# Kernel tuning notes

Measured on AMD Instinct MI355X. Metric: run time of the kernel, lower is better.

The kernel has to match this reference:

```python
import jax, jax.numpy as jnp
import numpy as np

B, S, D = 2, 1024, 768
H, HD = 12, 64
E, K, F = 8, 2, 3072
EPS = 1e-5


def _ln(x, g, b):
    mu = jnp.mean(x, -1, keepdims=True)
    var = jnp.mean(jnp.square(x - mu), -1, keepdims=True)
    return (x - mu) * jax.lax.rsqrt(var + EPS) * g + b


def setup_inputs() -> dict:
    key = jax.random.key(0)
    ks = jax.random.split(key, 12)
    s = lambda k, shape, sc: jax.random.normal(k, shape, jnp.float32) * sc
    return {
        "hidden_states": s(ks[0], (B, S, D), 1.0),
        "ln1_g": jnp.ones((D,), jnp.float32), "ln1_b": jnp.zeros((D,), jnp.float32),
        "w_attn": s(ks[1], (D, 3 * D), 0.02), "b_attn": jnp.zeros((3 * D,), jnp.float32),
        "w_attnproj": s(ks[2], (D, D), 0.02), "b_attnproj": jnp.zeros((D,), jnp.float32),
        "ln2_g": jnp.ones((D,), jnp.float32), "ln2_b": jnp.zeros((D,), jnp.float32),
        "w_router": s(ks[3], (E, D), 0.01),
        "w_fc": s(ks[4], (E, D, F), 0.02 / E), "b_fc": jnp.zeros((E, F), jnp.float32),
        "w_proj": s(ks[5], (E, F, D), 0.02 / E), "b_proj": jnp.zeros((E, D), jnp.float32),
    }


def reference(hidden_states, ln1_g, ln1_b, w_attn, b_attn, w_attnproj, b_attnproj,
              ln2_g, ln2_b, w_router, w_fc, b_fc, w_proj, b_proj):
    # --- attention sub-block (GPT-2 style, causal) ---
    residual = hidden_states
    x = _ln(hidden_states, ln1_g, ln1_b)
    qkv = x @ w_attn + b_attn                         # [B,S,3D]
    q, k, v = jnp.split(qkv, 3, axis=-1)
    def heads(t):
        return t.reshape(B, S, H, HD).transpose(0, 2, 1, 3)  # [B,H,S,HD]
    q, k, v = heads(q), heads(k), heads(v)
    scores = jnp.einsum("bhqd,bhkd->bhqk", q, k) / np.sqrt(HD).astype(np.float32)
    causal = jnp.tril(jnp.ones((S, S), bool))
    scores = jnp.where(causal, scores, jnp.finfo(scores.dtype).min)
    attn = jax.nn.softmax(scores, axis=-1)
    ctx = jnp.einsum("bhqk,bhkd->bhqd", attn, v)
    ctx = ctx.transpose(0, 2, 1, 3).reshape(B, S, D)
    attn_out = ctx @ w_attnproj + b_attnproj
    hs = attn_out + residual

    # --- MoE FFN sub-block ---
    residual = hs
    x2 = _ln(hs, ln2_g, ln2_b)
    logits = x2 @ w_router.T                          # [B,S,E]
    probs = jax.nn.softmax(logits, axis=-1)
    top_w, top_idx = jax.lax.top_k(probs, K)          # [B,S,K]
    top_w = top_w / jnp.sum(top_w, -1, keepdims=True)
    gates = jnp.sum(jax.nn.one_hot(top_idx, E, dtype=x2.dtype) * top_w[..., None], axis=2)  # [B,S,E]
    h = jax.nn.gelu(jnp.einsum("bsd,edf->bsef", x2, w_fc) + b_fc, approximate=False)
    y = jnp.einsum("bsef,efd->bsed", h, w_proj) + b_proj
    moe_out = jnp.einsum("bse,bsed->bsd", gates, y)
    return moe_out + residual
```

## Files before the change

kernel.cpp:

```cpp
#include <hip/hip_runtime.h>
#include <hip/hip_bf16.h>
#include <math.h>

#define NB 2
#define SEQ 1024
#define DM 768
#define NHEAD 12
#define HDIM 64
#define NEXP 8
#define FF 3072
#define NTOK (NB*SEQ)
#define TDIM (3*DM)
#define LNEPS 1e-5f
#define NSLOT (NTOK*2)

typedef __attribute__((ext_vector_type(8))) short v8s;
typedef __attribute__((ext_vector_type(4))) float v4f;

#define GLDS16(src, dst) \
    __builtin_amdgcn_global_load_lds((const __attribute__((address_space(1))) unsigned int*)(src), \
                                     (__attribute__((address_space(3))) unsigned int*)(dst), 16, 0, 0)

#define BARF() do { asm volatile("" ::: "memory"); __builtin_amdgcn_s_barrier(); asm volatile("" ::: "memory"); } while(0)
#define WAITV(n) asm volatile("s_waitcnt vmcnt(" #n ")" ::: "memory")

static __device__ __forceinline__ float bf2f(unsigned short u){
    return __uint_as_float(((unsigned)u) << 16);
}
static __device__ __forceinline__ unsigned short f2bf(float f){
    unsigned u = __float_as_uint(f);
    u += 0x7fffu + ((u >> 16) & 1u);
    return (unsigned short)(u >> 16);
}
static __device__ __forceinline__ float gelu_exact(float x){
    return 0.5f * x * (1.0f + erff(x * 0.70710678118654752440f));
}

__global__ __launch_bounds__(256) void tconv_kernel(const float* __restrict__ in,
                                                    unsigned short* __restrict__ out,
                                                    int R, int C){
    __shared__ float T[32][33];
    size_t base = (size_t)blockIdx.z * R * C;
    int c0 = blockIdx.x * 32, r0 = blockIdx.y * 32;
    int t = threadIdx.x;
    int tr = t >> 3, tc4 = (t & 7) * 4;
    float4 v = *(const float4*)&in[base + (size_t)(r0 + tr) * C + c0 + tc4];
    T[tr][tc4+0] = v.x; T[tr][tc4+1] = v.y; T[tr][tc4+2] = v.z; T[tr][tc4+3] = v.w;
    __syncthreads();
    int oc = t >> 3, or4 = (t & 7) * 4;
    ushort4 o;
    o.x = f2bf(T[or4+0][oc]); o.y = f2bf(T[or4+1][oc]);
    o.z = f2bf(T[or4+2][oc]); o.w = f2bf(T[or4+3][oc]);
    *(ushort4*)&out[base + (size_t)(c0 + oc) * R + r0 + or4] = o;
}

__global__ __launch_bounds__(256) void ln_b(const float* __restrict__ in,
                                            const float* __restrict__ g,
                                            const float* __restrict__ b,
                                            unsigned short* __restrict__ outb){
    int t = blockIdx.x;
    const float* row = in + (size_t)t * DM;
    int tid = threadIdx.x;
    float v0 = row[tid], v1 = row[tid + 256], v2 = row[tid + 512];
    float s  = v0 + v1 + v2;
    float ss = v0*v0 + v1*v1 + v2*v2;
    for (int off = 32; off; off >>= 1){
        s  += __shfl_down(s, off);
        ss += __shfl_down(ss, off);
    }
    __shared__ float ls[4], lss[4];
    int wid = tid >> 6, lane = tid & 63;
    if (lane == 0){ ls[wid] = s; lss[wid] = ss; }
    __syncthreads();
    if (tid == 0){
        float a = ls[0] + ls[1] + ls[2] + ls[3];
        float c = lss[0] + lss[1] + lss[2] + lss[3];
        float mu = a / (float)DM;
        float var = c / (float)DM - mu * mu;
        ls[0] = mu; lss[0] = rsqrtf(var + LNEPS);
    }
    __syncthreads();
    float mu = ls[0], rs = lss[0];
    unsigned short* obrow = outb + (size_t)t * DM;
    obrow[tid]     = f2bf((v0 - mu) * rs * g[tid]       + b[tid]);
    obrow[tid+256] = f2bf((v1 - mu) * rs * g[tid + 256] + b[tid + 256]);
    obrow[tid+512] = f2bf((v2 - mu) * rs * g[tid + 512] + b[tid + 512]);
}

__global__ __launch_bounds__(256) void ln_router(const float* __restrict__ in,
                                                 const float* __restrict__ g,
                                                 const float* __restrict__ b,
                                                 const float* __restrict__ wr,
                                                 unsigned short* __restrict__ outb,
                                                 int* __restrict__ cnt,
                                                 int* __restrict__ expTok,
                                                 int* __restrict__ tokE,
                                                 int* __restrict__ tokPos,
                                                 float* __restrict__ tokGate){
    int t = blockIdx.x;
    const float* row = in + (size_t)t * DM;
    int tid = threadIdx.x;
    float v0 = row[tid], v1 = row[tid + 256], v2 = row[tid + 512];
    float s  = v0 + v1 + v2;
    float ss = v0*v0 + v1*v1 + v2*v2;
    for (int off = 32; off; off >>= 1){
        s  += __shfl_down(s, off);
        ss += __shfl_down(ss, off);
    }
    __shared__ float ls[4], lss[4];
    __shared__ float wsum[4][NEXP];
    int wid = tid >> 6, lane = tid & 63;
    if (lane == 0){ ls[wid] = s; lss[wid] = ss; }
    __syncthreads();
    if (tid == 0){
        float a = ls[0] + ls[1] + ls[2] + ls[3];
        float c = lss[0] + lss[1] + lss[2] + lss[3];
        float mu = a / (float)DM;
        float var = c / (float)DM - mu * mu;
        ls[0] = mu; lss[0] = rsqrtf(var + LNEPS);
    }
    __syncthreads();
    float mu = ls[0], rs = lss[0];
    float o0 = (v0 - mu) * rs * g[tid]       + b[tid];
    float o1 = (v1 - mu) * rs * g[tid + 256] + b[tid + 256];
    float o2 = (v2 - mu) * rs * g[tid + 512] + b[tid + 512];
    unsigned short* obrow = outb + (size_t)t * DM;
    obrow[tid] = f2bf(o0); obrow[tid+256] = f2bf(o1); obrow[tid+512] = f2bf(o2);
    float p[NEXP];
    #pragma unroll
    for (int e = 0; e < NEXP; e++)
        p[e] = o0*wr[e*DM + tid] + o1*wr[e*DM + tid + 256] + o2*wr[e*DM + tid + 512];
    #pragma unroll
    for (int e = 0; e < NEXP; e++)
        for (int off = 32; off; off >>= 1) p[e] += __shfl_down(p[e], off);
    if (lane == 0){
        #pragma unroll
        for (int e = 0; e < NEXP; e++) wsum[wid][e] = p[e];
    }
    __syncthreads();
    if (tid == 0){
        float lg[NEXP];
        #pragma unroll
        for (int e = 0; e < NEXP; e++)
            lg[e] = wsum[0][e] + wsum[1][e] + wsum[2][e] + wsum[3][e];
        int i0 = 0; float m0 = lg[0];
        #pragma unroll
        for (int e = 1; e < NEXP; e++) if (lg[e] > m0){ m0 = lg[e]; i0 = e; }
        int i1 = -1; float m1 = -INFINITY;
        #pragma unroll
        for (int e = 0; e < NEXP; e++) if (e != i0 && lg[e] > m1){ m1 = lg[e]; i1 = e; }
        float mx = fmaxf(m0, m1);
        float e0 = __expf(m0 - mx), e1 = __expf(m1 - mx);
        float inv = 1.0f / (e0 + e1);
        int p0 = atomicAdd(&cnt[i0], 1);
        int p1 = atomicAdd(&cnt[i1], 1);
        expTok[i0*NTOK + p0] = t;
        expTok[i1*NTOK + p1] = t;
        tokE[t*2]   = i0; tokE[t*2+1]   = i1;
        tokPos[t*2] = p0; tokPos[t*2+1] = p1;
        tokGate[t*2]   = e0 * inv;
        tokGate[t*2+1] = e1 * inv;
    }
}

__global__ __launch_bounds__(256) void mm_qkv(const unsigned short* __restrict__ Ab,
                                              const unsigned short* __restrict__ Bb,
                                              const float* __restrict__ bias,
                                              unsigned short* __restrict__ Qb,
                                              unsigned short* __restrict__ Kb,
                                              unsigned short* __restrict__ Vt){
    __shared__ __align__(16) unsigned short As[2][64*32];
    __shared__ __align__(16) unsigned short Bs[2][64*32];
    int bm = blockIdx.y * 64, bn = blockIdx.x * 64;
    int tid = threadIdx.x, wave = tid >> 6, lane = tid & 63;
    int quad = lane >> 4, l15 = lane & 15;
    int wm = wave >> 1, wn = wave & 1;
    int arow = tid >> 2, achunk = (tid & 3) * 8;
    const unsigned short* aS = Ab + (size_t)(bm + arow) * DM + achunk;
    const unsigned short* bS = Bb + (size_t)(bn + arow) * DM + achunk;
    v4f acc[2][2];
    #pragma unroll
    for (int i = 0; i < 2; i++)
        #pragma unroll
        for (int j = 0; j < 2; j++) acc[i][j] = (v4f){0.f,0.f,0.f,0.f};

#define QKV_STAGE(buf, kt) do { int kb = (kt)*32; \
    GLDS16(aS + kb, &As[buf][(wave*16)*32]); \
    GLDS16(bS + kb, &Bs[buf][(wave*16)*32]); \
} while(0)
#define QKV_COMP(buf) do { \
    v8s a[2], bfr[2]; \
    _Pragma("unroll") \
    for (int i = 0; i < 2; i++){ \
        a[i]   = *(const v8s*)&As[buf][(wm*32 + i*16 + l15)*32 + quad*8]; \
        bfr[i] = *(const v8s*)&Bs[buf][(wn*32 + i*16 + l15)*32 + quad*8]; \
    } \
    _Pragma("unroll") \
    for (int mi = 0; mi < 2; mi++) \
        _Pragma("unroll") \
        for (int ni = 0; ni < 2; ni++) \
            acc[mi][ni] = __builtin_amdgcn_mfma_f32_16x16x32_bf16(a[mi], bfr[ni], acc[mi][ni], 0, 0, 0); \
} while(0)

    const int NK = DM/32;
    QKV_STAGE(0, 0);
    #pragma unroll 1
    for (int kt = 0; kt < NK; kt++){
        if (NK - kt > 1){ QKV_STAGE((kt+1)&1, kt+1); WAITV(2); }
        else            { WAITV(0); }
        BARF();
        QKV_COMP(kt&1);
        BARF();
    }
    int btyp = bn / DM;
    #pragma unroll
    for (int ni = 0; ni < 2; ni++){
        int n = bn + wn*32 + ni*16 + l15;
        float bb = bias[n];
        int hd = n % DM; int h = hd >> 6; int d = hd & 63;
        #pragma unroll
        for (int mi = 0; mi < 2; mi++){
            int m = bm + wm*32 + mi*16 + quad*4;
            int b = m >> 10, sd = m & 1023;
            size_t bhbase = (size_t)(b*NHEAD + h);
            if (btyp == 0){
                #pragma unroll
                for (int r = 0; r < 4; r++)
                    Qb[(bhbase*SEQ + sd + r)*HDIM + d] = f2bf((acc[mi][ni][r] + bb) * 0.125f);
            } else if (btyp == 1){
                #pragma unroll
                for (int r = 0; r < 4; r++)
                    Kb[(bhbase*SEQ + sd + r)*HDIM + d] = f2bf(acc[mi][ni][r] + bb);
            } else {
                ushort4 o;
                o.x = f2bf(acc[mi][ni][0] + bb); o.y = f2bf(acc[mi][ni][1] + bb);
                o.z = f2bf(acc[mi][ni][2] + bb); o.w = f2bf(acc[mi][ni][3] + bb);
                *(ushort4*)&Vt[(bhbase*HDIM + d)*SEQ + sd] = o;
            }
        }
    }
}

__global__ __launch_bounds__(64) void fattn(const unsigned short* __restrict__ Qb,
                                            const unsigned short* __restrict__ Kb,
                                            const unsigned short* __restrict__ Vt,
                                            unsigned short* __restrict__ ctxb){
    int bh = blockIdx.x >> 5;
    int q0 = (31 - (blockIdx.x & 31)) * 32;
    int h = bh % NHEAD, b = bh / NHEAD;
    int lane = threadIdx.x;
    int quad = lane >> 4, l15 = lane & 15;

    __shared__ __align__(16) unsigned short Plds[32*32];

    const unsigned short* qp = Qb + ((size_t)bh*SEQ + q0 + l15) * HDIM + quad*8;
    v8s qa00 = *(const v8s*)qp;
    v8s qa01 = *(const v8s*)(qp + 32);
    v8s qa10 = *(const v8s*)(qp + 16*HDIM);
    v8s qa11 = *(const v8s*)(qp + 16*HDIM + 32);

    v4f o[2][4];
    #pragma unroll
    for (int i = 0; i < 2; i++)
        #pragma unroll
        for (int j = 0; j < 4; j++) o[i][j] = (v4f){0.f,0.f,0.f,0.f};
    float mrow[2][4], lrow[2][4];
    #pragma unroll
    for (int i = 0; i < 2; i++)
        #pragma unroll
        for (int r = 0; r < 4; r++){ mrow[i][r] = -1e30f; lrow[i][r] = 0.f; }

    int nch = (q0 >> 5) + 1;
    for (int ch = 0; ch < nch; ch++){
        int kt = ch * 32;
        const unsigned short* kp = Kb + ((size_t)bh*SEQ + kt + l15) * HDIM + quad*8;
        v8s k00 = *(const v8s*)kp;
        v8s k01 = *(const v8s*)(kp + 32);
        v8s k10 = *(const v8s*)(kp + 16*HDIM);
        v8s k11 = *(const v8s*)(kp + 16*HDIM + 32);
        v4f s00 = {0,0,0,0}, s01 = {0,0,0,0}, s10 = {0,0,0,0}, s11 = {0,0,0,0};
        s00 = __builtin_amdgcn_mfma_f32_16x16x32_bf16(qa00, k00, s00, 0, 0, 0);
        s00 = __builtin_amdgcn_mfma_f32_16x16x32_bf16(qa01, k01, s00, 0, 0, 0);
        s01 = __builtin_amdgcn_mfma_f32_16x16x32_bf16(qa00, k10, s01, 0, 0, 0);
        s01 = __builtin_amdgcn_mfma_f32_16x16x32_bf16(qa01, k11, s01, 0, 0, 0);
        s10 = __builtin_amdgcn_mfma_f32_16x16x32_bf16(qa10, k00, s10, 0, 0, 0);
        s10 = __builtin_amdgcn_mfma_f32_16x16x32_bf16(qa11, k01, s10, 0, 0, 0);
        s11 = __builtin_amdgcn_mfma_f32_16x16x32_bf16(qa10, k10, s11, 0, 0, 0);
        s11 = __builtin_amdgcn_mfma_f32_16x16x32_bf16(qa11, k11, s11, 0, 0, 0);

        int key0 = kt + l15, key1 = kt + 16 + l15;
        float alpha[2][4];
        #pragma unroll
        for (int mi = 0; mi < 2; mi++){
            #pragma unroll
            for (int r = 0; r < 4; r++){
                int qrow = q0 + mi*16 + quad*4 + r;
                float sv0 = mi ? s10[r] : s00[r];
                float sv1 = mi ? s11[r] : s01[r];
                float v0 = (key0 <= qrow) ? sv0 : -1e30f;
                float v1 = (key1 <= qrow) ? sv1 : -1e30f;
                float mx = fmaxf(v0, v1);
                mx = fmaxf(mx, __shfl_xor(mx, 1));
                mx = fmaxf(mx, __shfl_xor(mx, 2));
                mx = fmaxf(mx, __shfl_xor(mx, 4));
                mx = fmaxf(mx, __shfl_xor(mx, 8));
                float mn = fmaxf(mrow[mi][r], mx);
                alpha[mi][r] = __expf(mrow[mi][r] - mn);
                float p0 = __expf(v0 - mn);
                float p1 = __expf(v1 - mn);
                float ps = p0 + p1;
                ps += __shfl_xor(ps, 1);
                ps += __shfl_xor(ps, 2);
                ps += __shfl_xor(ps, 4);
                ps += __shfl_xor(ps, 8);
                lrow[mi][r] = lrow[mi][r] * alpha[mi][r] + ps;
                mrow[mi][r] = mn;
                Plds[(mi*16 + quad*4 + r)*32 + l15]      = f2bf(p0);
                Plds[(mi*16 + quad*4 + r)*32 + 16 + l15] = f2bf(p1);
            }
        }
        #pragma unroll
        for (int mi = 0; mi < 2; mi++)
            #pragma unroll
            for (int df = 0; df < 4; df++)
                #pragma unroll
                for (int r = 0; r < 4; r++)
                    o[mi][df][r] *= alpha[mi][r];
        __syncthreads();
        v8s pa0 = *(const v8s*)&Plds[l15*32 + quad*8];
        v8s pa1 = *(const v8s*)&Plds[(16 + l15)*32 + quad*8];
        const unsigned short* vp = Vt + ((size_t)bh*HDIM + l15) * SEQ + kt + quad*8;
        #pragma unroll
        for (int df = 0; df < 4; df++){
            v8s vb = *(const v8s*)(vp + df*16*SEQ);
            o[0][df] = __builtin_amdgcn_mfma_f32_16x16x32_bf16(pa0, vb, o[0][df], 0, 0, 0);
            o[1][df] = __builtin_amdgcn_mfma_f32_16x16x32_bf16(pa1, vb, o[1][df], 0, 0, 0);
        }
        __syncthreads();
    }
    #pragma unroll
    for (int mi = 0; mi < 2; mi++){
        #pragma unroll
        for (int r = 0; r < 4; r++){
            float inv = 1.0f / lrow[mi][r];
            size_t orow = (size_t)(b*SEQ + q0 + mi*16 + quad*4 + r) * DM + h*HDIM;
            #pragma unroll
            for (int df = 0; df < 4; df++)
                ctxb[orow + df*16 + l15] = f2bf(o[mi][df][r] * inv);
        }
    }
}

__global__ __launch_bounds__(256) void mm_attnproj(const unsigned short* __restrict__ Ab,
                                                   const unsigned short* __restrict__ Bb,
                                                   const float* __restrict__ bias,
                                                   const float* __restrict__ res,
                                                   float* __restrict__ C){
    __shared__ __align__(16) unsigned short As[4][64*32];
    __shared__ __align__(16) unsigned short Bs[4][64*32];
    int bm = blockIdx.y * 64, bn = blockIdx.x * 64;
    int tid = threadIdx.x, wave = tid >> 6, lane = tid & 63;
    int quad = lane >> 4, l15 = lane & 15;
    int wm = wave >> 1, wn = wave & 1;
    int lrow = lane >> 2, lchunk = (lane & 3) * 8;
    const unsigned short* aS = Ab + (size_t)(bm + wave*16 + lrow) * DM + lchunk;
    const unsigned short* bS = Bb + (size_t)(bn + wave*16 + lrow) * DM + lchunk;
    v4f acc[2][2];
    #pragma unroll
    for (int i = 0; i < 2; i++)
        #pragma unroll
        for (int j = 0; j < 2; j++) acc[i][j] = (v4f){0.f,0.f,0.f,0.f};

#define AP_STAGE(buf, kt) do { int kb = (kt)*32; \
    GLDS16(aS + kb, &As[buf][(wave*16)*32]); \
    GLDS16(bS + kb, &Bs[buf][(wave*16)*32]); \
} while(0)
#define AP_COMP(buf) do { \
    v8s a[2], bfr[2]; \
    _Pragma("unroll") \
    for (int i = 0; i < 2; i++){ \
        a[i]   = *(const v8s*)&As[buf][(wm*32 + i*16 + l15)*32 + quad*8]; \
        bfr[i] = *(const v8s*)&Bs[buf][(wn*32 + i*16 + l15)*32 + quad*8]; \
    } \
    _Pragma("unroll") \
    for (int mi = 0; mi < 2; mi++) \
        _Pragma("unroll") \
        for (int ni = 0; ni < 2; ni++) \
            acc[mi][ni] = __builtin_amdgcn_mfma_f32_16x16x32_bf16(a[mi], bfr[ni], acc[mi][ni], 0, 0, 0); \
} while(0)

    const int NK = DM/32;
    AP_STAGE(0, 0); AP_STAGE(1, 1); AP_STAGE(2, 2);
    #pragma unroll 1
    for (int kt = 0; kt < NK; kt++){
        int rem = NK - kt;
        if (rem > 3){ AP_STAGE((kt+3)&3, kt+3); WAITV(6); }
        else if (rem == 3){ WAITV(4); }
        else if (rem == 2){ WAITV(2); }
        else { WAITV(0); }
        BARF();
        AP_COMP(kt&3);
        BARF();
    }
    #pragma unroll
    for (int ni = 0; ni < 2; ni++){
        int n = bn + wn*32 + ni*16 + l15;
        float bb = bias[n];
        #pragma unroll
        for (int mi = 0; mi < 2; mi++){
            int m = bm + wm*32 + mi*16 + quad*4;
            #pragma unroll
            for (int r = 0; r < 4; r++)
                C[(size_t)(m + r) * DM + n] = acc[mi][ni][r] + bb + res[(size_t)(m + r) * DM + n];
        }
    }
}

__global__ __launch_bounds__(256) void mm_fc(const unsigned short* __restrict__ Xb,
                                             const unsigned short* __restrict__ Wb,
                                             const float* __restrict__ bfc,
                                             const int* __restrict__ expTok,
                                             const int* __restrict__ cnt,
                                             const int* __restrict__ offE,
                                             unsigned short* __restrict__ H){
    int bid = blockIdx.x;
    int e = bid & 7;
    int t2 = bid >> 3;
    int tile = t2 & 31;
    int bn = (t2 >> 5) * 128;
    int c = cnt[e];
    int rows = c - tile * 64;
    if (rows <= 0) return;
    __shared__ __align__(16) unsigned short As[2][64*32];
    __shared__ __align__(16) unsigned short Bs[2][128*32];
    __shared__ int toks[64];
    int tid = threadIdx.x, wave = tid >> 6, lane = tid & 63;
    if (tid < 64){
        int idx = tile * 64 + tid;
        if (idx >= c) idx = c - 1;
        toks[tid] = expTok[e * NTOK + idx];
    }
    __syncthreads();
    int quad = lane >> 4, l15 = lane & 15;
    int wm = wave >> 1, wn = wave & 1;
    int lrow = lane >> 2;
    int pch = (((lane >> 3) & 3) ^ (lane & 3)) * 8;
    int tok0 = toks[wave*16 + lrow];
    const unsigned short* Be = Wb + (size_t)e * FF * DM;
    const unsigned short* aS  = Xb + (size_t)tok0 * DM + pch;
    const unsigned short* bS0 = Be + (size_t)(bn +      wave*16 + lrow) * DM + pch;
    const unsigned short* bS1 = Be + (size_t)(bn + 64 + wave*16 + lrow) * DM + pch;
    int q2 = (quad ^ ((l15 >> 1) & 3)) * 8;
    v4f acc[2][4];
    #pragma unroll
    for (int i = 0; i < 2; i++)
        #pragma unroll
        for (int j = 0; j < 4; j++) acc[i][j] = (v4f){0.f,0.f,0.f,0.f};

#define FC_STAGE(buf, kt) do { int kb = (kt)*32; \
    GLDS16(aS  + kb, &As[buf][(wave*16)*32]); \
    GLDS16(bS0 + kb, &Bs[buf][(     wave*16)*32]); \
    GLDS16(bS1 + kb, &Bs[buf][(64 + wave*16)*32]); \
} while(0)
#define FC_COMP(buf) do { \
    v8s a[2], bfr[4]; \
    _Pragma("unroll") \
    for (int i = 0; i < 2; i++) a[i] = *(const v8s*)&As[buf][(wm*32 + i*16 + l15)*32 + q2]; \
    _Pragma("unroll") \
    for (int i = 0; i < 4; i++) bfr[i] = *(const v8s*)&Bs[buf][(wn*64 + i*16 + l15)*32 + q2]; \
    _Pragma("unroll") \
    for (int mi = 0; mi < 2; mi++) \
        _Pragma("unroll") \
        for (int ni = 0; ni < 4; ni++) \
            acc[mi][ni] = __builtin_amdgcn_mfma_f32_16x16x32_bf16(a[mi], bfr[ni], acc[mi][ni], 0, 0, 0); \
} while(0)

    const int NK = DM/32;
    FC_STAGE(0, 0);
    #pragma unroll 1
    for (int kt = 0; kt < NK; kt++){
        if (NK - kt > 1){ FC_STAGE((kt+1)&1, kt+1); WAITV(3); }
        else            { WAITV(0); }
        BARF();
        FC_COMP(kt&1);
        BARF();
    }
    int slot0 = offE[e] + tile * 64;
    #pragma unroll
    for (int ni = 0; ni < 4; ni++){
        int n = bn + wn*64 + ni*16 + l15;
        float bb = bfc[(size_t)e * FF + n];
        #pragma unroll
        for (int mi = 0; mi < 2; mi++){
            int ml = wm*32 + mi*16 + quad*4;
            #pragma unroll
            for (int r = 0; r < 4; r++)
                if (ml + r < rows)
                    H[(size_t)(slot0 + ml + r) * FF + n] = f2bf(gelu_exact(acc[mi][ni][r] + bb));
        }
    }
}

__global__ __launch_bounds__(256) void mm_proj(const unsigned short* __restrict__ H,
                                               const unsigned short* __restrict__ Wb,
                                               const int* __restrict__ cnt,
                                               const int* __restrict__ offE,
                                               float* __restrict__ Yp){
    int bid = blockIdx.x;
    int e = bid & 7;
    int t2 = bid >> 3;
    int tile = t2 & 31;
    int xx = t2 >> 5;
    int sk = xx & 1;
    int bn = (xx >> 1) * 64;
    int c = cnt[e];
    int rows = c - tile * 64;
    if (rows <= 0) return;
    __shared__ __align__(16) unsigned short As[2][64*32];
    __shared__ __align__(16) unsigned short Bs[2][64*32];
    int tid = threadIdx.x, wave = tid >> 6, lane = tid & 63;
    int quad = lane >> 4, l15 = lane & 15;
    int wm = wave >> 1, wn = wave & 1;
    int slot0 = offE[e] + tile * 64;
    int arow = tid >> 2;
    int pch = (((lane >> 3) & 3) ^ (lane & 3)) * 8;
    int arl = arow < rows ? arow : rows - 1;
    const unsigned short* Be = Wb + (size_t)e * DM * FF;
    const unsigned short* aS = H  + (size_t)(slot0 + arl) * FF + sk*1536 + pch;
    const unsigned short* bS = Be + (size_t)(bn + arow) * FF + sk*1536 + pch;
    int q2 = (quad ^ ((l15 >> 1) & 3)) * 8;
    v4f acc[2][2];
    #pragma unroll
    for (int i = 0; i < 2; i++)
        #pragma unroll
        for (int j = 0; j < 2; j++) acc[i][j] = (v4f){0.f,0.f,0.f,0.f};

#define PJ_STAGE(buf, kt) do { int kb = (kt)*32; \
    GLDS16(aS + kb, &As[buf][(wave*16)*32]); \
    GLDS16(bS + kb, &Bs[buf][(wave*16)*32]); \
} while(0)
#define PJ_COMP(buf) do { \
    v8s a[2], bfr[2]; \
    _Pragma("unroll") \
    for (int i = 0; i < 2; i++){ \
        a[i]   = *(const v8s*)&As[buf][(wm*32 + i*16 + l15)*32 + q2]; \
        bfr[i] = *(const v8s*)&Bs[buf][(wn*32 + i*16 + l15)*32 + q2]; \
    } \
    _Pragma("unroll") \
    for (int mi = 0; mi < 2; mi++) \
        _Pragma("unroll") \
        for (int ni = 0; ni < 2; ni++) \
            acc[mi][ni] = __builtin_amdgcn_mfma_f32_16x16x32_bf16(a[mi], bfr[ni], acc[mi][ni], 0, 0, 0); \
} while(0)

    const int NK = 1536/32;
    PJ_STAGE(0, 0);
    #pragma unroll 1
    for (int kt = 0; kt < NK; kt++){
        if (NK - kt > 1){ PJ_STAGE((kt+1)&1, kt+1); WAITV(2); }
        else            { WAITV(0); }
        BARF();
        PJ_COMP(kt&1);
        BARF();
    }
    float* Yo = Yp + (size_t)sk * NSLOT * DM;
    #pragma unroll
    for (int ni = 0; ni < 2; ni++){
        int n = bn + wn*32 + ni*16 + l15;
        #pragma unroll
        for (int mi = 0; mi < 2; mi++){
            int ml = wm*32 + mi*16 + quad*4;
            #pragma unroll
            for (int r = 0; r < 4; r++)
                if (ml + r < rows)
                    Yo[(size_t)(slot0 + ml + r) * DM + n] = acc[mi][ni][r];
        }
    }
}

__global__ void offsets_kernel(const int* __restrict__ cnt, int* __restrict__ offE){
    if (threadIdx.x == 0 && blockIdx.x == 0){
        int a = 0;
        for (int e = 0; e < NEXP; e++){ offE[e] = a; a += cnt[e]; }
    }
}

__global__ __launch_bounds__(256) void combine_kernel(const float* __restrict__ hs,
                                                      const float* __restrict__ Yp,
                                                      const float* __restrict__ bproj,
                                                      const int* __restrict__ tokE,
                                                      const int* __restrict__ tokPos,
                                                      const float* __restrict__ tokGate,
                                                      const int* __restrict__ offE,
                                                      float* __restrict__ out){
    int t = blockIdx.x;
    int e0 = tokE[t*2], e1 = tokE[t*2+1];
    int s0 = offE[e0] + tokPos[t*2];
    int s1 = offE[e1] + tokPos[t*2+1];
    float g0 = tokGate[t*2], g1 = tokGate[t*2+1];
    const float* y0a = Yp + (size_t)s0 * DM;
    const float* y0b = Yp + (size_t)NSLOT * DM + (size_t)s0 * DM;
    const float* y1a = Yp + (size_t)s1 * DM;
    const float* y1b = Yp + (size_t)NSLOT * DM + (size_t)s1 * DM;
    const float* b0 = bproj + (size_t)e0 * DM;
    const float* b1 = bproj + (size_t)e1 * DM;
    const float* hr = hs + (size_t)t * DM;
    float* orow = out + (size_t)t * DM;
    for (int d = threadIdx.x; d < DM; d += 256){
        orow[d] = hr[d] + g0 * (y0a[d] + y0b[d] + b0[d]) + g1 * (y1a[d] + y1b[d] + b1[d]);
    }
}

extern "C" void kernel_launch(void* const* d_in, const int* in_sizes, int n_in,
                              void* d_out, int out_size, void* d_ws, size_t ws_size,
                              hipStream_t stream){
    (void)in_sizes; (void)n_in; (void)out_size; (void)ws_size;
    const float* hidden  = (const float*)d_in[0];
    const float* ln1_g   = (const float*)d_in[1];
    const float* ln1_b   = (const float*)d_in[2];
    const float* w_attn  = (const float*)d_in[3];
    const float* b_attn  = (const float*)d_in[4];
    const float* w_aproj = (const float*)d_in[5];
    const float* b_aproj = (const float*)d_in[6];
    const float* ln2_g   = (const float*)d_in[7];
    const float* ln2_b   = (const float*)d_in[8];
    const float* w_rout  = (const float*)d_in[9];
    const float* w_fc    = (const float*)d_in[10];
    const float* b_fc    = (const float*)d_in[11];
    const float* w_proj  = (const float*)d_in[12];
    const float* b_proj  = (const float*)d_in[13];
    float* out = (float*)d_out;

    char* ws = (char*)d_ws;
    float*          hs   = (float*)(ws + 0);
    unsigned short* xb   = (unsigned short*)(ws + 6291456);
    unsigned short* Qb   = (unsigned short*)(ws + 9437184);
    unsigned short* Kb   = (unsigned short*)(ws + 12582912);
    unsigned short* Vt   = (unsigned short*)(ws + 15728640);
    unsigned short* ctxb = (unsigned short*)(ws + 18874368);
    unsigned short* Wab  = (unsigned short*)(ws + 22020096);
    unsigned short* Wapb = (unsigned short*)(ws + 25559040);
    unsigned short* H    = (unsigned short*)(ws + 9437184);
    unsigned short* Wfcb = (unsigned short*)(ws + 34603008);
    unsigned short* Wprb = (unsigned short*)(ws + 72351744);
    float*          Yp   = (float*)(ws + 34603008);
    char* rt = ws + 110100480;
    int* cnt      = (int*)(rt + 0);
    int* offE     = (int*)(rt + 64);
    int* expTok   = (int*)(rt + 128);
    int* tokE     = (int*)(rt + 128 + 65536);
    int* tokPos   = (int*)(rt + 128 + 81920);
    float* tokGate= (float*)(rt + 128 + 98304);

    hipMemsetAsync(cnt, 0, NEXP * sizeof(int), stream);

    tconv_kernel<<<dim3(TDIM/32, DM/32, 1), 256, 0, stream>>>(w_attn, Wab, DM, TDIM);
    tconv_kernel<<<dim3(DM/32, DM/32, 1), 256, 0, stream>>>(w_aproj, Wapb, DM, DM);
    tconv_kernel<<<dim3(FF/32, DM/32, NEXP), 256, 0, stream>>>(w_fc, Wfcb, DM, FF);
    tconv_kernel<<<dim3(DM/32, FF/32, NEXP), 256, 0, stream>>>(w_proj, Wprb, FF, DM);

    ln_b<<<NTOK, 256, 0, stream>>>(hidden, ln1_g, ln1_b, xb);
    mm_qkv<<<dim3(TDIM/64, NTOK/64), 256, 0, stream>>>(xb, Wab, b_attn, Qb, Kb, Vt);
    fattn<<<NB*NHEAD*32, 64, 0, stream>>>(Qb, Kb, Vt, ctxb);
    mm_attnproj<<<dim3(DM/64, NTOK/64), 256, 0, stream>>>(ctxb, Wapb, b_aproj, hidden, hs);
    ln_router<<<NTOK, 256, 0, stream>>>(hs, ln2_g, ln2_b, w_rout, xb,
                                        cnt, expTok, tokE, tokPos, tokGate);
    offsets_kernel<<<1, 64, 0, stream>>>(cnt, offE);
    mm_fc<<<8 * (NTOK/64) * (FF/128), 256, 0, stream>>>(xb, Wfcb, b_fc, expTok, cnt, offE, H);
    mm_proj<<<8 * (NTOK/64) * ((DM/64)*2), 256, 0, stream>>>(H, Wprb, cnt, offE, Yp);
    combine_kernel<<<NTOK, 256, 0, stream>>>(hs, Yp, b_proj, tokE, tokPos, tokGate, offE, out);
}
```

Measured before the change: 496.6 us.

## Enlarge MoE FC and proj GEMM tiles to 256-row blocks with 512 threads

Rewrites the expert FC and projection GEMMs to use 256x256 (fc) and 256x128 (proj) block tiles with K-step 64, 8 waves per block, and an XOR-swizzled LDS layout. Token indices are now gathered directly per lane instead of through a shared toks array. The larger tiles raise arithmetic intensity and cut redundant weight and activation loads across blocks. In exchange, the kernels use much more LDS and more accumulator registers, and launch fewer blocks. That lowers occupancy and wastes work on partially filled 256-row expert tiles.

```diff
diff --git a/kernel.cpp b/kernel.cpp
--- a/kernel.cpp
+++ b/kernel.cpp
@@ -416,83 +416,88 @@
     }
 }
 
-__global__ __launch_bounds__(256) void mm_fc(const unsigned short* __restrict__ Xb,
-                                             const unsigned short* __restrict__ Wb,
-                                             const float* __restrict__ bfc,
-                                             const int* __restrict__ expTok,
-                                             const int* __restrict__ cnt,
-                                             const int* __restrict__ offE,
-                                             unsigned short* __restrict__ H){
+__global__ __launch_bounds__(512, 2) void mm_fc(const unsigned short* __restrict__ Xb,
+                                                const unsigned short* __restrict__ Wb,
+                                                const float* __restrict__ bfc,
+                                                const int* __restrict__ expTok,
+                                                const int* __restrict__ cnt,
+                                                const int* __restrict__ offE,
+                                                unsigned short* __restrict__ H){
     int bid = blockIdx.x;
     int e = bid & 7;
     int t2 = bid >> 3;
-    int tile = t2 & 31;
-    int bn = (t2 >> 5) * 128;
+    int mt = t2 & 7;
+    int bn = (t2 >> 3) * 256;
     int c = cnt[e];
-    int rows = c - tile * 64;
+    int rows = c - mt * 256;
     if (rows <= 0) return;
-    __shared__ __align__(16) unsigned short As[2][64*32];
-    __shared__ __align__(16) unsigned short Bs[2][128*32];
-    __shared__ int toks[64];
+    __shared__ __align__(16) unsigned short As[2][256*64];
+    __shared__ __align__(16) unsigned short Bs[2][256*64];
     int tid = threadIdx.x, wave = tid >> 6, lane = tid & 63;
-    if (tid < 64){
-        int idx = tile * 64 + tid;
-        if (idx >= c) idx = c - 1;
-        toks[tid] = expTok[e * NTOK + idx];
-    }
-    __syncthreads();
     int quad = lane >> 4, l15 = lane & 15;
-    int wm = wave >> 1, wn = wave & 1;
-    int lrow = lane >> 2;
-    int pch = (((lane >> 3) & 3) ^ (lane & 3)) * 8;
-    int tok0 = toks[wave*16 + lrow];
+    int wm = wave >> 2, wn = wave & 3;
+    int srow = lane >> 3;
+    int schunk = (lane & 7) ^ srow;
     const unsigned short* Be = Wb + (size_t)e * FF * DM;
-    const unsigned short* aS  = Xb + (size_t)tok0 * DM + pch;
-    const unsigned short* bS0 = Be + (size_t)(bn +      wave*16 + lrow) * DM + pch;
-    const unsigned short* bS1 = Be + (size_t)(bn + 64 + wave*16 + lrow) * DM + pch;
-    int q2 = (quad ^ ((l15 >> 1) & 3)) * 8;
-    v4f acc[2][4];
-    #pragma unroll
-    for (int i = 0; i < 2; i++)
+    const unsigned short* aSrc[4];
+    const unsigned short* bSrc[4];
+    #pragma unroll
+    for (int s = 0; s < 4; s++){
+        int arow = mt*256 + wave*32 + s*8 + srow;
+        if (arow >= c) arow = c - 1;
+        int tok = expTok[e*NTOK + arow];
+        aSrc[s] = Xb + (size_t)tok * DM + schunk*8;
+        bSrc[s] = Be + (size_t)(bn + wave*32 + s*8 + srow) * DM + schunk*8;
+    }
+    v4f acc[8][4];
+    #pragma unroll
+    for (int i = 0; i < 8; i++)
         #pragma unroll
         for (int j = 0; j < 4; j++) acc[i][j] = (v4f){0.f,0.f,0.f,0.f};
 
-#define FC_STAGE(buf, kt) do { int kb = (kt)*32; \
-    GLDS16(aS  + kb, &As[buf][(wave*16)*32]); \
-    GLDS16(bS0 + kb, &Bs[buf][(     wave*16)*32]); \
-    GLDS16(bS1 + kb, &Bs[buf][(64 + wave*16)*32]); \
-} while(0)
-#define FC_COMP(buf) do { \
-    v8s a[2], bfr[4]; \
-    _Pragma("unroll") \
-    for (int i = 0; i < 2; i++) a[i] = *(const v8s*)&As[buf][(wm*32 + i*16 + l15)*32 + q2]; \
-    _Pragma("unroll") \
-    for (int i = 0; i < 4; i++) bfr[i] = *(const v8s*)&Bs[buf][(wn*64 + i*16 + l15)*32 + q2]; \
-    _Pragma("unroll") \
-    for (int mi = 0; mi < 2; mi++) \
+#define FC_STG(buf, kt) do { int kb = (kt)*64; \
+    _Pragma("unroll") \
+    for (int s = 0; s < 4; s++){ \
+        GLDS16(aSrc[s] + kb, &As[buf][(wave*32 + s*8)*64]); \
+        GLDS16(bSrc[s] + kb, &Bs[buf][(wave*32 + s*8)*64]); \
+    } \
+} while(0)
+#define FC_CMP(buf) do { \
+    _Pragma("unroll") \
+    for (int h = 0; h < 2; h++){ \
+        v8s a[8], bq[4]; \
+        _Pragma("unroll") \
+        for (int mi = 0; mi < 8; mi++) \
+            a[mi] = *(const v8s*)&As[buf][(wm*128 + mi*16 + l15)*64 + ((h*4 + quad) ^ (l15 & 7))*8]; \
         _Pragma("unroll") \
         for (int ni = 0; ni < 4; ni++) \
-            acc[mi][ni] = __builtin_amdgcn_mfma_f32_16x16x32_bf16(a[mi], bfr[ni], acc[mi][ni], 0, 0, 0); \
-} while(0)
-
-    const int NK = DM/32;
-    FC_STAGE(0, 0);
+            bq[ni] = *(const v8s*)&Bs[buf][(wn*64 + ni*16 + l15)*64 + ((h*4 + quad) ^ (l15 & 7))*8]; \
+        _Pragma("unroll") \
+        for (int mi = 0; mi < 8; mi++) \
+            _Pragma("unroll") \
+            for (int ni = 0; ni < 4; ni++) \
+                acc[mi][ni] = __builtin_amdgcn_mfma_f32_16x16x32_bf16(a[mi], bq[ni], acc[mi][ni], 0, 0, 0); \
+    } \
+} while(0)
+
+    const int NK = DM/64;
+    FC_STG(0, 0);
     #pragma unroll 1
     for (int kt = 0; kt < NK; kt++){
-        if (NK - kt > 1){ FC_STAGE((kt+1)&1, kt+1); WAITV(3); }
+        if (kt + 1 < NK){ FC_STG((kt+1)&1, kt+1); WAITV(8); }
         else            { WAITV(0); }
         BARF();
-        FC_COMP(kt&1);
-        BARF();
-    }
-    int slot0 = offE[e] + tile * 64;
+        FC_CMP(kt&1);
+        BARF();
+    }
+    int slot0 = offE[e] + mt*256;
     #pragma unroll
     for (int ni = 0; ni < 4; ni++){
         int n = bn + wn*64 + ni*16 + l15;
         float bb = bfc[(size_t)e * FF + n];
         #pragma unroll
-        for (int mi = 0; mi < 2; mi++){
-            int ml = wm*32 + mi*16 + quad*4;
+        for (int mi = 0; mi < 8; mi++){
+            int ml = wm*128 + mi*16 + quad*4;
             #pragma unroll
             for (int r = 0; r < 4; r++)
                 if (ml + r < rows)
@@ -501,75 +506,90 @@
     }
 }
 
-__global__ __launch_bounds__(256) void mm_proj(const unsigned short* __restrict__ H,
-                                               const unsigned short* __restrict__ Wb,
-                                               const int* __restrict__ cnt,
-                                               const int* __restrict__ offE,
-                                               float* __restrict__ Yp){
+__global__ __launch_bounds__(512, 2) void mm_proj(const unsigned short* __restrict__ H,
+                                                  const unsigned short* __restrict__ Wb,
+                                                  const int* __restrict__ cnt,
+                                                  const int* __restrict__ offE,
+                                                  float* __restrict__ Yp){
     int bid = blockIdx.x;
     int e = bid & 7;
     int t2 = bid >> 3;
-    int tile = t2 & 31;
-    int xx = t2 >> 5;
-    int sk = xx & 1;
-    int bn = (xx >> 1) * 64;
+    int mt = t2 & 7;
+    int t3 = t2 >> 3;
+    int sk = t3 & 1;
+    int bn = (t3 >> 1) * 128;
     int c = cnt[e];
-    int rows = c - tile * 64;
+    int rows = c - mt * 256;
     if (rows <= 0) return;
-    __shared__ __align__(16) unsigned short As[2][64*32];
-    __shared__ __align__(16) unsigned short Bs[2][64*32];
+    __shared__ __align__(16) unsigned short As[2][256*64];
+    __shared__ __align__(16) unsigned short Bs[2][128*64];
     int tid = threadIdx.x, wave = tid >> 6, lane = tid & 63;
     int quad = lane >> 4, l15 = lane & 15;
     int wm = wave >> 1, wn = wave & 1;
-    int slot0 = offE[e] + tile * 64;
-    int arow = tid >> 2;
-    int pch = (((lane >> 3) & 3) ^ (lane & 3)) * 8;
-    int arl = arow < rows ? arow : rows - 1;
+    int slot0 = offE[e] + mt*256;
+    int srow = lane >> 3;
+    int schunk = (lane & 7) ^ srow;
     const unsigned short* Be = Wb + (size_t)e * DM * FF;
-    const unsigned short* aS = H  + (size_t)(slot0 + arl) * FF + sk*1536 + pch;
-    const unsigned short* bS = Be + (size_t)(bn + arow) * FF + sk*1536 + pch;
-    int q2 = (quad ^ ((l15 >> 1) & 3)) * 8;
-    v4f acc[2][2];
-    #pragma unroll
-    for (int i = 0; i < 2; i++)
-        #pragma unroll
-        for (int j = 0; j < 2; j++) acc[i][j] = (v4f){0.f,0.f,0.f,0.f};
-
-#define PJ_STAGE(buf, kt) do { int kb = (kt)*32; \
-    GLDS16(aS + kb, &As[buf][(wave*16)*32]); \
-    GLDS16(bS + kb, &Bs[buf][(wave*16)*32]); \
-} while(0)
-#define PJ_COMP(buf) do { \
-    v8s a[2], bfr[2]; \
-    _Pragma("unroll") \
-    for (int i = 0; i < 2; i++){ \
-        a[i]   = *(const v8s*)&As[buf][(wm*32 + i*16 + l15)*32 + q2]; \
-        bfr[i] = *(const v8s*)&Bs[buf][(wn*32 + i*16 + l15)*32 + q2]; \
+    const unsigned short* aSrc[4];
+    const unsigned short* bSrc[2];
+    #pragma unroll
+    for (int s = 0; s < 4; s++){
+        int arow = wave*32 + s*8 + srow;
+        if (arow >= rows) arow = rows - 1;
+        aSrc[s] = H + (size_t)(slot0 + arow) * FF + sk*1536 + schunk*8;
+    }
+    #pragma unroll
+    for (int s = 0; s < 2; s++)
+        bSrc[s] = Be + (size_t)(bn + wave*16 + s*8 + srow) * FF + sk*1536 + schunk*8;
+    v4f acc[4][4];
+    #pragma unroll
+    for (int i = 0; i < 4; i++)
+        #pragma unroll
+        for (int j = 0; j < 4; j++) acc[i][j] = (v4f){0.f,0.f,0.f,0.f};
+
+#define PJ_STG(buf, kt) do { int kb = (kt)*64; \
+    _Pragma("unroll") \
+    for (int s = 0; s < 4; s++) \
+        GLDS16(aSrc[s] + kb, &As[buf][(wave*32 + s*8)*64]); \
+    _Pragma("unroll") \
+    for (int s = 0; s < 2; s++) \
+        GLDS16(bSrc[s] + kb, &Bs[buf][(wave*16 + s*8)*64]); \
+} while(0)
+#define PJ_CMP(buf) do { \
+    _Pragma("unroll") \
+    for (int h = 0; h < 2; h++){ \
+        v8s a[4], bq[4]; \
+        _Pragma("unroll") \
+        for (int mi = 0; mi < 4; mi++) \
+            a[mi] = *(const v8s*)&As[buf][(wm*64 + mi*16 + l15)*64 + ((h*4 + quad) ^ (l15 & 7))*8]; \
+        _Pragma("unroll") \
+        for (int ni = 0; ni < 4; ni++) \
+            bq[ni] = *(const v8s*)&Bs[buf][(wn*64 + ni*16 + l15)*64 + ((h*4 + quad) ^ (l15 & 7))*8]; \
+        _Pragma("unroll") \
+        for (int mi = 0; mi < 4; mi++) \
+            _Pragma("unroll") \
+            for (int ni = 0; ni < 4; ni++) \
+                acc[mi][ni] = __builtin_amdgcn_mfma_f32_16x16x32_bf16(a[mi], bq[ni], acc[mi][ni], 0, 0, 0); \
     } \
-    _Pragma("unroll") \
-    for (int mi = 0; mi < 2; mi++) \
-        _Pragma("unroll") \
-        for (int ni = 0; ni < 2; ni++) \
-            acc[mi][ni] = __builtin_amdgcn_mfma_f32_16x16x32_bf16(a[mi], bfr[ni], acc[mi][ni], 0, 0, 0); \
-} while(0)
-
-    const int NK = 1536/32;
-    PJ_STAGE(0, 0);
+} while(0)
+
+    const int NK = 1536/64;
+    PJ_STG(0, 0);
     #pragma unroll 1
     for (int kt = 0; kt < NK; kt++){
-        if (NK - kt > 1){ PJ_STAGE((kt+1)&1, kt+1); WAITV(2); }
+        if (kt + 1 < NK){ PJ_STG((kt+1)&1, kt+1); WAITV(6); }
         else            { WAITV(0); }
         BARF();
-        PJ_COMP(kt&1);
+        PJ_CMP(kt&1);
         BARF();
     }
     float* Yo = Yp + (size_t)sk * NSLOT * DM;
     #pragma unroll
-    for (int ni = 0; ni < 2; ni++){
-        int n = bn + wn*32 + ni*16 + l15;
-        #pragma unroll
-        for (int mi = 0; mi < 2; mi++){
-            int ml = wm*32 + mi*16 + quad*4;
+    for (int ni = 0; ni < 4; ni++){
+        int n = bn + wn*64 + ni*16 + l15;
+        #pragma unroll
+        for (int mi = 0; mi < 4; mi++){
+            int ml = wm*64 + mi*16 + quad*4;
             #pragma unroll
             for (int r = 0; r < 4; r++)
                 if (ml + r < rows)
@@ -666,7 +686,7 @@
     ln_router<<<NTOK, 256, 0, stream>>>(hs, ln2_g, ln2_b, w_rout, xb,
                                         cnt, expTok, tokE, tokPos, tokGate);
     offsets_kernel<<<1, 64, 0, stream>>>(cnt, offE);
-    mm_fc<<<8 * (NTOK/64) * (FF/128), 256, 0, stream>>>(xb, Wfcb, b_fc, expTok, cnt, offE, H);
-    mm_proj<<<8 * (NTOK/64) * ((DM/64)*2), 256, 0, stream>>>(H, Wprb, cnt, offE, Yp);
+    mm_fc<<<8 * 8 * (FF/256), 512, 0, stream>>>(xb, Wfcb, b_fc, expTok, cnt, offE, H);
+    mm_proj<<<8 * 8 * 2 * (DM/128), 512, 0, stream>>>(H, Wprb, cnt, offE, Yp);
     combine_kernel<<<NTOK, 256, 0, stream>>>(hs, Yp, b_proj, tokE, tokPos, tokGate, offE, out);
 }
```

Result: slower. 534.2 us (+7.6%).
